# Kernel tuning notes

Hardware: AMD Instinct MI355X
Metric: run time of the kernel (lower is better)

## Reference

```python
import jax, jax.numpy as jnp
import numpy as np

NB_OBJECTS = 3
DIM_BODY = 10
DIM_OBJECT = 15
DIM_ACT = 4
DIM_NODE = 128
D_PHI_IN = DIM_ACT + DIM_BODY + DIM_OBJECT + DIM_NODE  # 157
HID = 256
D_PHI_OUT = 3 * D_PHI_IN  # 471
D_RHO_OUT = 1
BATCH = 65536


def _linear_init(key, fan_in, fan_out):
    # torch nn.Linear default: U(-1/sqrt(fan_in), 1/sqrt(fan_in))
    bound = 1.0 / np.sqrt(fan_in)
    k1, k2 = jax.random.split(key)
    W = jax.random.uniform(k1, (fan_in, fan_out), minval=-bound, maxval=bound, dtype=jnp.float32)
    b = jax.random.uniform(k2, (fan_out,), minval=-bound, maxval=bound, dtype=jnp.float32)
    return W, b


def setup_inputs() -> dict:
    key = jax.random.key(0)
    ks = jax.random.split(key, 11)
    obs = jax.random.normal(ks[0], (BATCH, DIM_BODY + NB_OBJECTS * DIM_OBJECT), dtype=jnp.float32)
    act = jax.random.normal(ks[1], (BATCH, DIM_ACT), dtype=jnp.float32)
    nodes = jax.random.normal(ks[2], (NB_OBJECTS, BATCH, DIM_NODE), dtype=jnp.float32)
    phi1_w1, phi1_b1 = _linear_init(ks[3], D_PHI_IN, HID)
    phi1_w2, phi1_b2 = _linear_init(ks[4], HID, D_PHI_OUT)
    phi2_w1, phi2_b1 = _linear_init(ks[5], D_PHI_IN, HID)
    phi2_w2, phi2_b2 = _linear_init(ks[6], HID, D_PHI_OUT)
    rho1_w1, rho1_b1 = _linear_init(ks[7], D_PHI_OUT, HID)
    rho1_w2, rho1_b2 = _linear_init(ks[8], HID, D_RHO_OUT)
    rho2_w1, rho2_b1 = _linear_init(ks[9], D_PHI_OUT, HID)
    rho2_w2, rho2_b2 = _linear_init(ks[10], HID, D_RHO_OUT)
    return {
        "obs": obs, "act": act, "nodes": nodes,
        "phi1_w1": phi1_w1, "phi1_b1": phi1_b1, "phi1_w2": phi1_w2, "phi1_b2": phi1_b2,
        "phi2_w1": phi2_w1, "phi2_b1": phi2_b1, "phi2_w2": phi2_w2, "phi2_b2": phi2_b2,
        "rho1_w1": rho1_w1, "rho1_b1": rho1_b1, "rho1_w2": rho1_w2, "rho1_b2": rho1_b2,
        "rho2_w1": rho2_w1, "rho2_b1": rho2_b1, "rho2_w2": rho2_w2, "rho2_b2": rho2_b2,
    }


def reference(obs, act, nodes,
              phi1_w1, phi1_b1, phi1_w2, phi1_b2,
              phi2_w1, phi2_b1, phi2_w2, phi2_b2,
              rho1_w1, rho1_b1, rho1_w2, rho1_b2,
              rho2_w1, rho2_b1, rho2_w2, rho2_b2):
    B = obs.shape[0]
    obs_body = obs[:, :DIM_BODY]                                   # [B, 10]
    # per-object slices -> [nb_objects, B, dim_object]
    obs_obj = obs[:, DIM_BODY:].reshape(B, NB_OBJECTS, DIM_OBJECT).transpose(1, 0, 2)
    shared = jnp.concatenate([act, obs_body], axis=-1)             # [B, 14]
    shared = jnp.broadcast_to(shared[None], (NB_OBJECTS, B, shared.shape[-1]))
    inp_phi = jnp.concatenate([shared, obs_obj, nodes], axis=-1)   # [3, B, 157]

    def mlp2(x, w1, b1, w2, b2):
        h = jax.nn.relu(x @ w1 + b1)
        return jax.nn.relu(h @ w2 + b2)

    # DeepSet: per-entity phi then sum over entities
    out1 = mlp2(inp_phi, phi1_w1, phi1_b1, phi1_w2, phi1_b2).sum(axis=0)  # [B, 471]
    out2 = mlp2(inp_phi, phi2_w1, phi2_b1, phi2_w2, phi2_b2).sum(axis=0)
    q1 = jax.nn.relu(out1 @ rho1_w1 + rho1_b1) @ rho1_w2 + rho1_b2        # [B, 1]
    q2 = jax.nn.relu(out2 @ rho2_w1 + rho2_b1) @ rho2_w2 + rho2_b2
    return (q1, q2)
```

## Files before the change

### kernel.cpp

```cpp
#include <hip/hip_runtime.h>
#include <hip/hip_fp16.h>

typedef _Float16 half8 __attribute__((ext_vector_type(8)));
typedef float f32x4 __attribute__((ext_vector_type(4)));

#define BATCH 65536
#define M1 196608
#define K1 192

#define GLL16(g, l) __builtin_amdgcn_global_load_lds( \
    (const __attribute__((address_space(1))) unsigned int*)(const void*)(g), \
    (__attribute__((address_space(3))) unsigned int*)(void*)(l), 16, 0, 0)

__global__ void prep_kernel(const float* __restrict__ p1w1, const float* __restrict__ p2w1,
                            const float* __restrict__ p1w2, const float* __restrict__ p2w2,
                            const float* __restrict__ r1w1, const float* __restrict__ r2w1,
                            const float* __restrict__ p1b1, const float* __restrict__ p2b1,
                            const float* __restrict__ p1b2, const float* __restrict__ p2b2,
                            const float* __restrict__ rb1a, const float* __restrict__ rb1b,
                            _Float16* __restrict__ W1t, _Float16* __restrict__ W2t,
                            _Float16* __restrict__ R1t, float* __restrict__ b1cat,
                            float* __restrict__ b2cat, float* __restrict__ rbias) {
    int e = blockIdx.x * 256 + threadIdx.x;
    if (e < 98304) {
        int n = e / 192, c = e % 192;
        int k = (c < 128) ? (29 + c) : (c - 128);
        float v = 0.f;
        if (c < 128 || (c - 128) < 29) v = (n < 256) ? p1w1[k * 256 + n] : p2w1[k * 256 + (n - 256)];
        W1t[e] = (_Float16)v;
        return;
    }
    e -= 98304;
    if (e < 262144) {
        int net = e >> 17, rr = e & 131071;
        int n = rr >> 8, k = rr & 255;
        const float* w = net ? p2w2 : p1w2;
        W2t[(size_t)net * 131072 + rr] = (n < 471) ? (_Float16)w[k * 471 + n] : (_Float16)0.f;
        return;
    }
    e -= 262144;
    if (e < 262144) {
        int net = e >> 17, rr = e & 131071;
        int n = rr >> 9, k = rr & 511;
        const float* w = net ? r2w1 : r1w1;
        R1t[(size_t)net * 131072 + rr] = (k < 471) ? (_Float16)w[k * 256 + n] : (_Float16)0.f;
        return;
    }
    e -= 262144;
    if (e < 512) { b1cat[e] = (e < 256) ? p1b1[e] : p2b1[e - 256]; return; }
    e -= 512;
    if (e < 1024) {
        int net = e >> 9, n = e & 511;
        b2cat[e] = (n < 471) ? (net ? p2b2 : p1b2)[n] : 0.f;
        return;
    }
    e -= 1024;
    if (e < 512) {
        int net = e >> 8, n = e & 255;
        rbias[e] = (net ? rb1b : rb1a)[n];
    }
}

__global__ void build_x(const float* __restrict__ obs, const float* __restrict__ act,
                        const float* __restrict__ nodes, _Float16* __restrict__ Xh) {
    long idx = (long)blockIdx.x * 256 + threadIdx.x;
    int ch = (int)(idx % 24);
    long r = idx / 24;
    int o = (int)(r >> 16), b = (int)(r & 65535);
    half8 v;
    if (ch < 16) {
        const float* s = nodes + r * 128 + ch * 8;
#pragma unroll
        for (int j = 0; j < 8; ++j) v[j] = (_Float16)s[j];
    } else if (ch < 20) {
#pragma unroll
        for (int j = 0; j < 8; ++j) {
            int lc = ch * 8 + j - 128;
            float f = 0.f;
            if (lc < 4)       f = act[b * 4 + lc];
            else if (lc < 14) f = obs[b * 55 + (lc - 4)];
            else if (lc < 29) f = obs[b * 55 + 10 + o * 15 + (lc - 14)];
            v[j] = (_Float16)f;
        }
    } else {
#pragma unroll
        for (int j = 0; j < 8; ++j) v[j] = (_Float16)0.f;
    }
    *(half8*)(Xh + r * 192 + ch * 8) = v;
}

__global__ __launch_bounds__(512) void gemm1(const _Float16* __restrict__ Xh,
                                             const _Float16* __restrict__ W1t,
                                             const float* __restrict__ b1cat,
                                             _Float16* __restrict__ H) {
    __shared__ _Float16 As[2][8192];
    __shared__ _Float16 Bs[2][8192];
    const int tid = threadIdx.x;
    int bid = blockIdx.x;
    int w = (bid & 7) * 768 + (bid >> 3);
    const int m0 = (w >> 2) * 128, n0 = (w & 3) * 128;
    const _Float16* Ab = Xh + (long)m0 * K1;
    const _Float16* Bb = W1t + (long)n0 * K1;
    const int wid = tid >> 6, lane = tid & 63;
    const int lm = lane & 15, lq = lane >> 4;
    const int wr = (wid >> 2) * 64, wc = (wid & 3) * 32;
    const int xv = lm & 7;

#pragma unroll
    for (int t = 0; t < 2; ++t) {
        int c = t * 512 + tid, row = c >> 3, q = (c & 7) ^ (row & 7);
        GLL16(Ab + (long)row * K1 + q * 8, &As[0][0] + t * 4096 + wid * 512);
        GLL16(Bb + (long)row * K1 + q * 8, &Bs[0][0] + t * 4096 + wid * 512);
    }
    __syncthreads();

    f32x4 acc[4][2] = {};
    int cur = 0;
    for (int r = 0; r < 3; ++r) {
        if (r < 2) {
            int ko = (r + 1) * 64;
            _Float16* dA = &As[cur ^ 1][0];
            _Float16* dB = &Bs[cur ^ 1][0];
#pragma unroll
            for (int t = 0; t < 2; ++t) {
                int c = t * 512 + tid, row = c >> 3, q = (c & 7) ^ (row & 7);
                GLL16(Ab + (long)row * K1 + ko + q * 8, dA + t * 4096 + wid * 512);
                GLL16(Bb + (long)row * K1 + ko + q * 8, dB + t * 4096 + wid * 512);
            }
        }
        const _Float16* ab = &As[cur][0];
        const _Float16* bb = &Bs[cur][0];
#pragma unroll
        for (int ks = 0; ks < 2; ++ks) {
            const int off = ((ks * 4 + lq) ^ xv) * 8;
            half8 a[4], b[2];
#pragma unroll
            for (int i = 0; i < 4; ++i) a[i] = *(const half8*)(ab + (wr + i * 16 + lm) * 64 + off);
#pragma unroll
            for (int j = 0; j < 2; ++j) b[j] = *(const half8*)(bb + (wc + j * 16 + lm) * 64 + off);
#pragma unroll
            for (int i = 0; i < 4; ++i)
#pragma unroll
                for (int j = 0; j < 2; ++j)
                    acc[i][j] = __builtin_amdgcn_mfma_f32_16x16x32_f16(a[i], b[j], acc[i][j], 0, 0, 0);
        }
        __syncthreads();
        cur ^= 1;
    }
#pragma unroll
    for (int j = 0; j < 2; ++j) {
        int n = n0 + wc + j * 16 + lm;
        int net = n >> 8, ncol = n & 255;
        float bi = b1cat[n];
        _Float16* hp = H + (long)net * ((long)M1 * 256) + ncol;
#pragma unroll
        for (int i = 0; i < 4; ++i) {
            int mrow = m0 + wr + i * 16 + lq * 4;
#pragma unroll
            for (int rg = 0; rg < 4; ++rg) {
                float v = acc[i][j][rg] + bi;
                v = v > 0.f ? v : 0.f;
                hp[(long)(mrow + rg) * 256] = (_Float16)v;
            }
        }
    }
}

__global__ __launch_bounds__(512) void gemm_sum(const _Float16* __restrict__ H,
                                                const _Float16* __restrict__ W2t,
                                                const float* __restrict__ b2cat,
                                                _Float16* __restrict__ Osum) {
    __shared__ _Float16 As[2][8192];
    __shared__ _Float16 Bs[2][8192];
    const int tid = threadIdx.x;
    int bid = blockIdx.x;
    int w = (bid & 7) * 512 + (bid >> 3);
    const int b0 = (w >> 3) * 128;
    const int sub = w & 7;
    const int n0 = (sub & 3) * 128, net = sub >> 2;
    const _Float16* Ab = H + (long)net * ((long)M1 * 256) + (long)b0 * 256;
    const _Float16* Bb = W2t + (long)net * 131072 + (long)n0 * 256;
    const float* bp = b2cat + net * 512;
    const int wid = tid >> 6, lane = tid & 63;
    const int lm = lane & 15, lq = lane >> 4;
    const int wr = (wid >> 2) * 64, wc = (wid & 3) * 32;
    const int xv = lm & 7;

    float bi[2];
#pragma unroll
    for (int j = 0; j < 2; ++j) bi[j] = bp[n0 + wc + j * 16 + lm];

#pragma unroll
    for (int t = 0; t < 2; ++t) {
        int c = t * 512 + tid, row = c >> 3, q = (c & 7) ^ (row & 7);
        GLL16(Ab + (long)row * 256 + q * 8, &As[0][0] + t * 4096 + wid * 512);
        GLL16(Bb + (long)row * 256 + q * 8, &Bs[0][0] + t * 4096 + wid * 512);
    }
    __syncthreads();

    f32x4 accA[4][2] = {};
    f32x4 sum[4][2] = {};
    int cur = 0;
    for (int r = 0; r < 12; ++r) {
        if (r < 11) {
            int rn = r + 1;
            int obj = rn >> 2, ko = (rn & 3) * 64;
            _Float16* dA = &As[cur ^ 1][0];
            _Float16* dB = &Bs[cur ^ 1][0];
#pragma unroll
            for (int t = 0; t < 2; ++t) {
                int c = t * 512 + tid, row = c >> 3, q = (c & 7) ^ (row & 7);
                GLL16(Ab + ((long)obj * BATCH + row) * 256 + ko + q * 8, dA + t * 4096 + wid * 512);
                GLL16(Bb + (long)row * 256 + ko + q * 8, dB + t * 4096 + wid * 512);
            }
        }
        const _Float16* ab = &As[cur][0];
        const _Float16* bb = &Bs[cur][0];
#pragma unroll
        for (int ks = 0; ks < 2; ++ks) {
            const int off = ((ks * 4 + lq) ^ xv) * 8;
            half8 a[4], b[2];
#pragma unroll
            for (int i = 0; i < 4; ++i) a[i] = *(const half8*)(ab + (wr + i * 16 + lm) * 64 + off);
#pragma unroll
            for (int j = 0; j < 2; ++j) b[j] = *(const half8*)(bb + (wc + j * 16 + lm) * 64 + off);
#pragma unroll
            for (int i = 0; i < 4; ++i)
#pragma unroll
                for (int j = 0; j < 2; ++j)
                    accA[i][j] = __builtin_amdgcn_mfma_f32_16x16x32_f16(a[i], b[j], accA[i][j], 0, 0, 0);
        }
        if ((r & 3) == 3) {
#pragma unroll
            for (int i = 0; i < 4; ++i)
#pragma unroll
                for (int j = 0; j < 2; ++j) {
#pragma unroll
                    for (int rg = 0; rg < 4; ++rg) {
                        float v = accA[i][j][rg] + bi[j];
                        sum[i][j][rg] += (v > 0.f ? v : 0.f);
                    }
                    accA[i][j] = f32x4{0.f, 0.f, 0.f, 0.f};
                }
        }
        __syncthreads();
        cur ^= 1;
    }
    _Float16* op = Osum + (long)net * ((long)BATCH * 512);
#pragma unroll
    for (int j = 0; j < 2; ++j) {
        int n = n0 + wc + j * 16 + lm;
#pragma unroll
        for (int i = 0; i < 4; ++i) {
            int mrow = b0 + wr + i * 16 + lq * 4;
#pragma unroll
            for (int rg = 0; rg < 4; ++rg)
                op[(long)(mrow + rg) * 512 + n] = (_Float16)sum[i][j][rg];
        }
    }
}

__global__ __launch_bounds__(512) void gemm3q(const _Float16* __restrict__ Osum,
                                              const _Float16* __restrict__ R1t,
                                              const float* __restrict__ rbias,
                                              const float* __restrict__ r1w2,
                                              const float* __restrict__ r2w2,
                                              const float* __restrict__ r1b2,
                                              const float* __restrict__ r2b2,
                                              float* __restrict__ out) {
    __shared__ _Float16 As[2][8192];
    __shared__ _Float16 Bs[2][16384];
    __shared__ float qlds[128];
    const int tid = threadIdx.x;
    const int b0 = blockIdx.x * 128, net = blockIdx.z;
    if (tid < 128) qlds[tid] = 0.f;
    const _Float16* Ab = Osum + (long)net * ((long)BATCH * 512) + (long)b0 * 512;
    const _Float16* Bb = R1t + (long)net * 131072;
    const int wid = tid >> 6, lane = tid & 63;
    const int lm = lane & 15, lq = lane >> 4;
    const int wr = (wid >> 2) * 64, wc = (wid & 3) * 64;
    const int xv = lm & 7;

#pragma unroll
    for (int t = 0; t < 2; ++t) {
        int c = t * 512 + tid, row = c >> 3, q = (c & 7) ^ (row & 7);
        GLL16(Ab + (long)row * 512 + q * 8, &As[0][0] + t * 4096 + wid * 512);
    }
#pragma unroll
    for (int t = 0; t < 4; ++t) {
        int c = t * 512 + tid, row = c >> 3, q = (c & 7) ^ (row & 7);
        GLL16(Bb + (long)row * 512 + q * 8, &Bs[0][0] + t * 4096 + wid * 512);
    }
    __syncthreads();

    f32x4 acc[4][4] = {};
    int cur = 0;
    for (int r = 0; r < 8; ++r) {
        if (r < 7) {
            int ko = (r + 1) * 64;
            _Float16* dA = &As[cur ^ 1][0];
            _Float16* dB = &Bs[cur ^ 1][0];
#pragma unroll
            for (int t = 0; t < 2; ++t) {
                int c = t * 512 + tid, row = c >> 3, q = (c & 7) ^ (row & 7);
                GLL16(Ab + (long)row * 512 + ko + q * 8, dA + t * 4096 + wid * 512);
            }
#pragma unroll
            for (int t = 0; t < 4; ++t) {
                int c = t * 512 + tid, row = c >> 3, q = (c & 7) ^ (row & 7);
                GLL16(Bb + (long)row * 512 + ko + q * 8, dB + t * 4096 + wid * 512);
            }
        }
        const _Float16* ab = &As[cur][0];
        const _Float16* bb = &Bs[cur][0];
#pragma unroll
        for (int ks = 0; ks < 2; ++ks) {
            const int off = ((ks * 4 + lq) ^ xv) * 8;
            half8 a[4], b[4];
#pragma unroll
            for (int i = 0; i < 4; ++i) a[i] = *(const half8*)(ab + (wr + i * 16 + lm) * 64 + off);
#pragma unroll
            for (int j = 0; j < 4; ++j) b[j] = *(const half8*)(bb + (wc + j * 16 + lm) * 64 + off);
#pragma unroll
            for (int i = 0; i < 4; ++i)
#pragma unroll
                for (int j = 0; j < 4; ++j)
                    acc[i][j] = __builtin_amdgcn_mfma_f32_16x16x32_f16(a[i], b[j], acc[i][j], 0, 0, 0);
        }
        __syncthreads();
        cur ^= 1;
    }
    const float* w2 = net ? r2w2 : r1w2;
    const float* rb = rbias + net * 256;
    float w2v[4], bv[4];
#pragma unroll
    for (int j = 0; j < 4; ++j) {
        int col = wc + j * 16 + lm;
        w2v[j] = w2[col];
        bv[j] = rb[col];
    }
    f32x4 qp[4] = {};
#pragma unroll
    for (int i = 0; i < 4; ++i)
#pragma unroll
        for (int j = 0; j < 4; ++j)
#pragma unroll
            for (int rg = 0; rg < 4; ++rg) {
                float v = acc[i][j][rg] + bv[j];
                v = v > 0.f ? v : 0.f;
                qp[i][rg] += v * w2v[j];
            }
#pragma unroll
    for (int d = 1; d < 16; d <<= 1)
#pragma unroll
        for (int i = 0; i < 4; ++i)
#pragma unroll
            for (int rg = 0; rg < 4; ++rg)
                qp[i][rg] += __shfl_xor(qp[i][rg], d, 64);
    if ((lane & 15) == 0) {
#pragma unroll
        for (int i = 0; i < 4; ++i)
#pragma unroll
            for (int rg = 0; rg < 4; ++rg)
                atomicAdd(&qlds[wr + i * 16 + lq * 4 + rg], qp[i][rg]);
    }
    __syncthreads();
    if (tid < 128)
        out[(long)net * BATCH + b0 + tid] = qlds[tid] + (net ? r2b2[0] : r1b2[0]);
}

extern "C" void kernel_launch(void* const* d_in, const int* in_sizes, int n_in,
                              void* d_out, int out_size, void* d_ws, size_t ws_size,
                              hipStream_t stream) {
    const float* obs  = (const float*)d_in[0];
    const float* act  = (const float*)d_in[1];
    const float* nodes= (const float*)d_in[2];
    const float* p1w1 = (const float*)d_in[3];  const float* p1b1 = (const float*)d_in[4];
    const float* p1w2 = (const float*)d_in[5];  const float* p1b2 = (const float*)d_in[6];
    const float* p2w1 = (const float*)d_in[7];  const float* p2b1 = (const float*)d_in[8];
    const float* p2w2 = (const float*)d_in[9];  const float* p2b2 = (const float*)d_in[10];
    const float* r1w1 = (const float*)d_in[11]; const float* r1b1 = (const float*)d_in[12];
    const float* r1w2 = (const float*)d_in[13]; const float* r1b2 = (const float*)d_in[14];
    const float* r2w1 = (const float*)d_in[15]; const float* r2b1 = (const float*)d_in[16];
    const float* r2w2 = (const float*)d_in[17]; const float* r2b2 = (const float*)d_in[18];

    const size_t oW1t  = 0;
    const size_t oW2t  = 196608;
    const size_t oR1t  = 720896;
    const size_t oB1   = 1245184;
    const size_t oB2   = 1247232;
    const size_t oRB   = 1251328;
    const size_t oXO   = 1253376;
    const size_t oH    = 135471104;
    const size_t need  = 336797696;
    if (ws_size < need) return;

    char* ws = (char*)d_ws;
    _Float16* W1t  = (_Float16*)(ws + oW1t);
    _Float16* W2t  = (_Float16*)(ws + oW2t);
    _Float16* R1t  = (_Float16*)(ws + oR1t);
    float*    b1cat= (float*)(ws + oB1);
    float*    b2cat= (float*)(ws + oB2);
    float*    rbias= (float*)(ws + oRB);
    _Float16* Xh   = (_Float16*)(ws + oXO);
    _Float16* Osum = (_Float16*)(ws + oXO);
    _Float16* H    = (_Float16*)(ws + oH);
    float* out = (float*)d_out;

    prep_kernel<<<2440, 256, 0, stream>>>(p1w1, p2w1, p1w2, p2w2, r1w1, r2w1,
                                          p1b1, p2b1, p1b2, p2b2, r1b1, r2b1,
                                          W1t, W2t, R1t, b1cat, b2cat, rbias);
    build_x<<<18432, 256, 0, stream>>>(obs, act, nodes, Xh);
    gemm1<<<6144, 512, 0, stream>>>(Xh, W1t, b1cat, H);
    gemm_sum<<<4096, 512, 0, stream>>>(H, W2t, b2cat, Osum);
    gemm3q<<<dim3(512, 1, 2), 512, 0, stream>>>(Osum, R1t, rbias, r1w2, r2w2, r1b2, r2b2, out);
}
```

Baseline: 330.8 us.

## Triple-buffer GEMM pipelines with vmcnt waits and widen tiles to 128x256

All three GEMM kernels move from double-buffered LDS with __syncthreads to a three-stage ring. Each stage is waited on with explicit s_waitcnt vmcnt and a raw s_barrier, so two loads stay in flight while compute runs. gemm1 and gemm_sum widen the N tile from 128 to 256, which doubles the MFMA work per A load and halves the grid. gemm3q switches to a swizzled 1D grid. The cost is more LDS (about 144KB per block) and more accumulator registers, which lowers occupancy and relies on the manual vmcnt counts being right.

New measurement: 346.8 us. 4.8% more time.

```diff
diff --git a/kernel.cpp b/kernel.cpp
--- a/kernel.cpp
+++ b/kernel.cpp
@@ -11,6 +11,9 @@
 #define GLL16(g, l) __builtin_amdgcn_global_load_lds( \
     (const __attribute__((address_space(1))) unsigned int*)(const void*)(g), \
     (__attribute__((address_space(3))) unsigned int*)(void*)(l), 16, 0, 0)
+
+#define WAIT_VM(N) asm volatile("s_waitcnt vmcnt(" #N ")" ::: "memory")
+#define SBAR() do { __builtin_amdgcn_s_barrier(); __builtin_amdgcn_sched_barrier(0); } while (0)
 
 __global__ void prep_kernel(const float* __restrict__ p1w1, const float* __restrict__ p2w1,
                             const float* __restrict__ p1w2, const float* __restrict__ p2w2,
@@ -89,66 +92,67 @@
     *(half8*)(Xh + r * 192 + ch * 8) = v;
 }
 
+
 __global__ __launch_bounds__(512) void gemm1(const _Float16* __restrict__ Xh,
                                              const _Float16* __restrict__ W1t,
                                              const float* __restrict__ b1cat,
                                              _Float16* __restrict__ H) {
-    __shared__ _Float16 As[2][8192];
-    __shared__ _Float16 Bs[2][8192];
+    __shared__ _Float16 As[3][8192];
+    __shared__ _Float16 Bs[3][16384];
     const int tid = threadIdx.x;
     int bid = blockIdx.x;
-    int w = (bid & 7) * 768 + (bid >> 3);
-    const int m0 = (w >> 2) * 128, n0 = (w & 3) * 128;
+    int w = (bid & 7) * 384 + (bid >> 3);
+    const int m0 = (w >> 1) * 128, n0 = (w & 1) * 256;
     const _Float16* Ab = Xh + (long)m0 * K1;
     const _Float16* Bb = W1t + (long)n0 * K1;
     const int wid = tid >> 6, lane = tid & 63;
     const int lm = lane & 15, lq = lane >> 4;
-    const int wr = (wid >> 2) * 64, wc = (wid & 3) * 32;
+    const int wr = (wid >> 2) * 64, wc = (wid & 3) * 64;
     const int xv = lm & 7;
-
-#pragma unroll
-    for (int t = 0; t < 2; ++t) {
-        int c = t * 512 + tid, row = c >> 3, q = (c & 7) ^ (row & 7);
-        GLL16(Ab + (long)row * K1 + q * 8, &As[0][0] + t * 4096 + wid * 512);
-        GLL16(Bb + (long)row * K1 + q * 8, &Bs[0][0] + t * 4096 + wid * 512);
-    }
-    __syncthreads();
-
-    f32x4 acc[4][2] = {};
-    int cur = 0;
+    const int srow = tid >> 3, schk = tid & 7;
+
+    auto stage = [&](int s, _Float16* dA, _Float16* dB) {
+        int ko = s * 64;
+#pragma unroll
+        for (int g = 0; g < 2; ++g) {
+            int row = srow + g * 64, q = schk ^ (row & 7);
+            GLL16(Ab + (long)row * K1 + ko + q * 8, dA + g * 4096 + wid * 512);
+        }
+#pragma unroll
+        for (int g = 0; g < 4; ++g) {
+            int row = srow + g * 64, q = schk ^ (row & 7);
+            GLL16(Bb + (long)row * K1 + ko + q * 8, dB + g * 4096 + wid * 512);
+        }
+    };
+
+    stage(0, &As[0][0], &Bs[0][0]);
+    stage(1, &As[1][0], &Bs[1][0]);
+
+    f32x4 acc[4][4] = {};
+#pragma unroll
     for (int r = 0; r < 3; ++r) {
-        if (r < 2) {
-            int ko = (r + 1) * 64;
-            _Float16* dA = &As[cur ^ 1][0];
-            _Float16* dB = &Bs[cur ^ 1][0];
-#pragma unroll
-            for (int t = 0; t < 2; ++t) {
-                int c = t * 512 + tid, row = c >> 3, q = (c & 7) ^ (row & 7);
-                GLL16(Ab + (long)row * K1 + ko + q * 8, dA + t * 4096 + wid * 512);
-                GLL16(Bb + (long)row * K1 + ko + q * 8, dB + t * 4096 + wid * 512);
-            }
-        }
-        const _Float16* ab = &As[cur][0];
-        const _Float16* bb = &Bs[cur][0];
+        if (r < 2) { WAIT_VM(6); } else { WAIT_VM(0); }
+        SBAR();
+        if (r + 2 < 3) stage(r + 2, &As[(r + 2) % 3][0], &Bs[(r + 2) % 3][0]);
+        const _Float16* ab = &As[r % 3][0];
+        const _Float16* bb = &Bs[r % 3][0];
 #pragma unroll
         for (int ks = 0; ks < 2; ++ks) {
             const int off = ((ks * 4 + lq) ^ xv) * 8;
-            half8 a[4], b[2];
+            half8 a[4], b[4];
 #pragma unroll
             for (int i = 0; i < 4; ++i) a[i] = *(const half8*)(ab + (wr + i * 16 + lm) * 64 + off);
 #pragma unroll
-            for (int j = 0; j < 2; ++j) b[j] = *(const half8*)(bb + (wc + j * 16 + lm) * 64 + off);
+            for (int j = 0; j < 4; ++j) b[j] = *(const half8*)(bb + (wc + j * 16 + lm) * 64 + off);
 #pragma unroll
             for (int i = 0; i < 4; ++i)
 #pragma unroll
-                for (int j = 0; j < 2; ++j)
+                for (int j = 0; j < 4; ++j)
                     acc[i][j] = __builtin_amdgcn_mfma_f32_16x16x32_f16(a[i], b[j], acc[i][j], 0, 0, 0);
         }
-        __syncthreads();
-        cur ^= 1;
-    }
-#pragma unroll
-    for (int j = 0; j < 2; ++j) {
+    }
+#pragma unroll
+    for (int j = 0; j < 4; ++j) {
         int n = n0 + wc + j * 16 + lm;
         int net = n >> 8, ncol = n & 255;
         float bi = b1cat[n];
@@ -170,85 +174,83 @@
                                                 const _Float16* __restrict__ W2t,
                                                 const float* __restrict__ b2cat,
                                                 _Float16* __restrict__ Osum) {
-    __shared__ _Float16 As[2][8192];
-    __shared__ _Float16 Bs[2][8192];
+    __shared__ _Float16 As[3][8192];
+    __shared__ _Float16 Bs[3][16384];
     const int tid = threadIdx.x;
     int bid = blockIdx.x;
-    int w = (bid & 7) * 512 + (bid >> 3);
-    const int b0 = (w >> 3) * 128;
-    const int sub = w & 7;
-    const int n0 = (sub & 3) * 128, net = sub >> 2;
+    int w = (bid & 7) * 256 + (bid >> 3);
+    const int ncol = w & 1, net = (w >> 1) & 1, b0 = (w >> 2) * 128;
+    const int n0 = ncol * 256;
     const _Float16* Ab = H + (long)net * ((long)M1 * 256) + (long)b0 * 256;
     const _Float16* Bb = W2t + (long)net * 131072 + (long)n0 * 256;
     const float* bp = b2cat + net * 512;
     const int wid = tid >> 6, lane = tid & 63;
     const int lm = lane & 15, lq = lane >> 4;
-    const int wr = (wid >> 2) * 64, wc = (wid & 3) * 32;
+    const int wr = (wid >> 2) * 64, wc = (wid & 3) * 64;
     const int xv = lm & 7;
-
-    float bi[2];
-#pragma unroll
-    for (int j = 0; j < 2; ++j) bi[j] = bp[n0 + wc + j * 16 + lm];
-
-#pragma unroll
-    for (int t = 0; t < 2; ++t) {
-        int c = t * 512 + tid, row = c >> 3, q = (c & 7) ^ (row & 7);
-        GLL16(Ab + (long)row * 256 + q * 8, &As[0][0] + t * 4096 + wid * 512);
-        GLL16(Bb + (long)row * 256 + q * 8, &Bs[0][0] + t * 4096 + wid * 512);
-    }
-    __syncthreads();
-
-    f32x4 accA[4][2] = {};
-    f32x4 sum[4][2] = {};
-    int cur = 0;
+    const int srow = tid >> 3, schk = tid & 7;
+
+    float bi[4];
+#pragma unroll
+    for (int j = 0; j < 4; ++j) bi[j] = bp[n0 + wc + j * 16 + lm];
+
+    auto stage = [&](int s, _Float16* dA, _Float16* dB) {
+        int obj = s >> 2, ko = (s & 3) * 64;
+#pragma unroll
+        for (int g = 0; g < 2; ++g) {
+            int row = srow + g * 64, q = schk ^ (row & 7);
+            GLL16(Ab + ((long)obj * BATCH + row) * 256 + ko + q * 8, dA + g * 4096 + wid * 512);
+        }
+#pragma unroll
+        for (int g = 0; g < 4; ++g) {
+            int row = srow + g * 64, q = schk ^ (row & 7);
+            GLL16(Bb + (long)row * 256 + ko + q * 8, dB + g * 4096 + wid * 512);
+        }
+    };
+
+    stage(0, &As[0][0], &Bs[0][0]);
+    stage(1, &As[1][0], &Bs[1][0]);
+
+    f32x4 acc[4][4] = {};
+    f32x4 sum[4][4] = {};
+#pragma unroll
     for (int r = 0; r < 12; ++r) {
-        if (r < 11) {
-            int rn = r + 1;
-            int obj = rn >> 2, ko = (rn & 3) * 64;
-            _Float16* dA = &As[cur ^ 1][0];
-            _Float16* dB = &Bs[cur ^ 1][0];
-#pragma unroll
-            for (int t = 0; t < 2; ++t) {
-                int c = t * 512 + tid, row = c >> 3, q = (c & 7) ^ (row & 7);
-                GLL16(Ab + ((long)obj * BATCH + row) * 256 + ko + q * 8, dA + t * 4096 + wid * 512);
-                GLL16(Bb + (long)row * 256 + ko + q * 8, dB + t * 4096 + wid * 512);
-            }
-        }
-        const _Float16* ab = &As[cur][0];
-        const _Float16* bb = &Bs[cur][0];
+        if (r < 11) { WAIT_VM(6); } else { WAIT_VM(0); }
+        SBAR();
+        if (r + 2 < 12) stage(r + 2, &As[(r + 2) % 3][0], &Bs[(r + 2) % 3][0]);
+        const _Float16* ab = &As[r % 3][0];
+        const _Float16* bb = &Bs[r % 3][0];
 #pragma unroll
         for (int ks = 0; ks < 2; ++ks) {
             const int off = ((ks * 4 + lq) ^ xv) * 8;
-            half8 a[4], b[2];
+            half8 a[4], b[4];
 #pragma unroll
             for (int i = 0; i < 4; ++i) a[i] = *(const half8*)(ab + (wr + i * 16 + lm) * 64 + off);
 #pragma unroll
-            for (int j = 0; j < 2; ++j) b[j] = *(const half8*)(bb + (wc + j * 16 + lm) * 64 + off);
+            for (int j = 0; j < 4; ++j) b[j] = *(const half8*)(bb + (wc + j * 16 + lm) * 64 + off);
 #pragma unroll
             for (int i = 0; i < 4; ++i)
 #pragma unroll
-                for (int j = 0; j < 2; ++j)
-                    accA[i][j] = __builtin_amdgcn_mfma_f32_16x16x32_f16(a[i], b[j], accA[i][j], 0, 0, 0);
+                for (int j = 0; j < 4; ++j)
+                    acc[i][j] = __builtin_amdgcn_mfma_f32_16x16x32_f16(a[i], b[j], acc[i][j], 0, 0, 0);
         }
         if ((r & 3) == 3) {
 #pragma unroll
             for (int i = 0; i < 4; ++i)
 #pragma unroll
-                for (int j = 0; j < 2; ++j) {
+                for (int j = 0; j < 4; ++j) {
 #pragma unroll
                     for (int rg = 0; rg < 4; ++rg) {
-                        float v = accA[i][j][rg] + bi[j];
+                        float v = acc[i][j][rg] + bi[j];
                         sum[i][j][rg] += (v > 0.f ? v : 0.f);
                     }
-                    accA[i][j] = f32x4{0.f, 0.f, 0.f, 0.f};
+                    acc[i][j] = f32x4{0.f, 0.f, 0.f, 0.f};
                 }
         }
-        __syncthreads();
-        cur ^= 1;
     }
     _Float16* op = Osum + (long)net * ((long)BATCH * 512);
 #pragma unroll
-    for (int j = 0; j < 2; ++j) {
+    for (int j = 0; j < 4; ++j) {
         int n = n0 + wc + j * 16 + lm;
 #pragma unroll
         for (int i = 0; i < 4; ++i) {
@@ -268,11 +270,13 @@
                                               const float* __restrict__ r1b2,
                                               const float* __restrict__ r2b2,
                                               float* __restrict__ out) {
-    __shared__ _Float16 As[2][8192];
-    __shared__ _Float16 Bs[2][16384];
+    __shared__ _Float16 As[3][8192];
+    __shared__ _Float16 Bs[3][16384];
     __shared__ float qlds[128];
     const int tid = threadIdx.x;
-    const int b0 = blockIdx.x * 128, net = blockIdx.z;
+    int bid = blockIdx.x;
+    int w = (bid & 7) * 128 + (bid >> 3);
+    const int net = w & 1, b0 = (w >> 1) * 128;
     if (tid < 128) qlds[tid] = 0.f;
     const _Float16* Ab = Osum + (long)net * ((long)BATCH * 512) + (long)b0 * 512;
     const _Float16* Bb = R1t + (long)net * 131072;
@@ -280,39 +284,33 @@
     const int lm = lane & 15, lq = lane >> 4;
     const int wr = (wid >> 2) * 64, wc = (wid & 3) * 64;
     const int xv = lm & 7;
-
-#pragma unroll
-    for (int t = 0; t < 2; ++t) {
-        int c = t * 512 + tid, row = c >> 3, q = (c & 7) ^ (row & 7);
-        GLL16(Ab + (long)row * 512 + q * 8, &As[0][0] + t * 4096 + wid * 512);
-    }
-#pragma unroll
-    for (int t = 0; t < 4; ++t) {
-        int c = t * 512 + tid, row = c >> 3, q = (c & 7) ^ (row & 7);
-        GLL16(Bb + (long)row * 512 + q * 8, &Bs[0][0] + t * 4096 + wid * 512);
-    }
-    __syncthreads();
+    const int srow = tid >> 3, schk = tid & 7;
+
+    auto stage = [&](int s, _Float16* dA, _Float16* dB) {
+        int ko = s * 64;
+#pragma unroll
+        for (int g = 0; g < 2; ++g) {
+            int row = srow + g * 64, q = schk ^ (row & 7);
+            GLL16(Ab + (long)row * 512 + ko + q * 8, dA + g * 4096 + wid * 512);
+        }
+#pragma unroll
+        for (int g = 0; g < 4; ++g) {
+            int row = srow + g * 64, q = schk ^ (row & 7);
+            GLL16(Bb + (long)row * 512 + ko + q * 8, dB + g * 4096 + wid * 512);
+        }
+    };
+
+    stage(0, &As[0][0], &Bs[0][0]);
+    stage(1, &As[1][0], &Bs[1][0]);
 
     f32x4 acc[4][4] = {};
-    int cur = 0;
+#pragma unroll
     for (int r = 0; r < 8; ++r) {
-        if (r < 7) {
-            int ko = (r + 1) * 64;
-            _Float16* dA = &As[cur ^ 1][0];
-            _Float16* dB = &Bs[cur ^ 1][0];
-#pragma unroll
-            for (int t = 0; t < 2; ++t) {
-                int c = t * 512 + tid, row = c >> 3, q = (c & 7) ^ (row & 7);
-                GLL16(Ab + (long)row * 512 + ko + q * 8, dA + t * 4096 + wid * 512);
-            }
-#pragma unroll
-            for (int t = 0; t < 4; ++t) {
-                int c = t * 512 + tid, row = c >> 3, q = (c & 7) ^ (row & 7);
-                GLL16(Bb + (long)row * 512 + ko + q * 8, dB + t * 4096 + wid * 512);
-            }
-        }
-        const _Float16* ab = &As[cur][0];
-        const _Float16* bb = &Bs[cur][0];
+        if (r < 7) { WAIT_VM(6); } else { WAIT_VM(0); }
+        SBAR();
+        if (r + 2 < 8) stage(r + 2, &As[(r + 2) % 3][0], &Bs[(r + 2) % 3][0]);
+        const _Float16* ab = &As[r % 3][0];
+        const _Float16* bb = &Bs[r % 3][0];
 #pragma unroll
         for (int ks = 0; ks < 2; ++ks) {
             const int off = ((ks * 4 + lq) ^ xv) * 8;
@@ -327,8 +325,6 @@
                 for (int j = 0; j < 4; ++j)
                     acc[i][j] = __builtin_amdgcn_mfma_f32_16x16x32_f16(a[i], b[j], acc[i][j], 0, 0, 0);
         }
-        __syncthreads();
-        cur ^= 1;
     }
     const float* w2 = net ? r2w2 : r1w2;
     const float* rb = rbias + net * 256;
@@ -411,7 +407,7 @@
                                           p1b1, p2b1, p1b2, p2b2, r1b1, r2b1,
                                           W1t, W2t, R1t, b1cat, b2cat, rbias);
     build_x<<<18432, 256, 0, stream>>>(obs, act, nodes, Xh);
-    gemm1<<<6144, 512, 0, stream>>>(Xh, W1t, b1cat, H);
-    gemm_sum<<<4096, 512, 0, stream>>>(H, W2t, b2cat, Osum);
-    gemm3q<<<dim3(512, 1, 2), 512, 0, stream>>>(Osum, R1t, rbias, r1w2, r2w2, r1b2, r2b2, out);
-}
+    gemm1<<<3072, 512, 0, stream>>>(Xh, W1t, b1cat, H);
+    gemm_sum<<<2048, 512, 0, stream>>>(H, W2t, b2cat, Osum);
+    gemm3q<<<1024, 512, 0, stream>>>(Osum, R1t, rbias, r1w2, r2w2, r1b2, r2b2, out);
+}
```
